# Optimization experiments

Measured on AMD Instinct MI355X. Metric: run time of the kernel, lower is better.

Reference implementation:

```python
import jax, jax.numpy as jnp
import numpy as np


def setup_inputs() -> dict:
    key = jax.random.key(0)
    k1, k2, k3, k4, k5 = jax.random.split(key, 5)
    B, NODES, HID, C, H, W = 16, 64, 128, 256, 128, 128
    inp = {
        "input": jax.random.normal(k1, (1, B, NODES, HID), dtype=jnp.float32),
        "res_feature": jax.random.normal(k2, (B, C, H, W), dtype=jnp.float32),
        "node_fea_for_res": jax.random.normal(k3, (C, 1), dtype=jnp.float32) * 0.05,
        "node_fea_for_hidden": jax.random.normal(k4, (HID, 1), dtype=jnp.float32) * 0.05,
        "weight": jax.random.normal(k5, (HID, C), dtype=jnp.float32) * 0.05,
    }
    return inp


def reference(input, res_feature, node_fea_for_res, node_fea_for_hidden, weight):
    # input: (1, B, nodes, hidden); res_feature: (B, C, H, W)
    b, c, h, w = res_feature.shape
    x = input[0]  # (B, nodes, hidden)

    # res_feature -> (B, HW, C)
    res = res_feature.reshape(b, c, h * w).transpose(0, 2, 1)

    # The torch code expands to (B, HW, nodes, C/hidden) before the matmuls,
    # but the results are constant along the broadcast axis, so compute the
    # reduced projections once and broadcast-add.
    s_res = (res @ node_fea_for_res)[:, :, 0]        # (B, HW)
    s_hid = (x @ node_fea_for_hidden)[:, :, 0]       # (B, nodes)
    scores = s_res[:, :, None] + s_hid[:, None, :]   # (B, HW, nodes)

    attn = jax.nn.softmax(scores, axis=-1)           # softmax over nodes
    new_weight = x @ weight                          # (B, nodes, C)
    feature_out = jnp.einsum('bpn,bnc->bpc', attn, new_weight)  # (B, HW, C)

    feature_out = feature_out.transpose(0, 2, 1).reshape(b, c, h, w)
    return jax.nn.relu(feature_out)
```

## Files before the change

### kernel.cpp

```cpp
#include <hip/hip_runtime.h>

#define BB    16
#define NODES 64
#define HID   128
#define CC    256
#define HWP   16384

__global__ __launch_bounds__(256) void attn_vec_kernel(
    const float* __restrict__ x,
    const float* __restrict__ nfh,
    const float* __restrict__ w,
    float*       __restrict__ vals)
{
    __shared__ float s_part[NODES][4];
    __shared__ float attn[NODES];
    __shared__ float y[HID];

    const int b   = blockIdx.x;
    const int tid = threadIdx.x;

    {
        const int n = tid >> 2;
        const int q = tid & 3;
        const float* xp = x + ((size_t)b * NODES + n) * HID + q * 32;
        const float* fp = nfh + q * 32;
        float acc = 0.f;
        #pragma unroll
        for (int k = 0; k < 32; ++k) acc = fmaf(xp[k], fp[k], acc);
        s_part[n][q] = acc;
    }
    __syncthreads();

    if (tid < NODES) {
        float v = s_part[tid][0] + s_part[tid][1] + s_part[tid][2] + s_part[tid][3];
        float m = v;
        #pragma unroll
        for (int off = 32; off >= 1; off >>= 1)
            m = fmaxf(m, __shfl_xor(m, off, 64));
        float e = __expf(v - m);
        float ssum = e;
        #pragma unroll
        for (int off = 32; off >= 1; off >>= 1)
            ssum += __shfl_xor(ssum, off, 64);
        attn[tid] = e / ssum;
    }
    __syncthreads();

    if (tid < HID) {
        const float* xb = x + (size_t)b * NODES * HID + tid;
        float acc = 0.f;
        #pragma unroll 8
        for (int n = 0; n < NODES; ++n)
            acc = fmaf(attn[n], xb[(size_t)n * HID], acc);
        y[tid] = acc;
    }
    __syncthreads();

    {
        float acc = 0.f;
        #pragma unroll 8
        for (int k = 0; k < HID; ++k)
            acc = fmaf(y[k], w[(size_t)k * CC + tid], acc);
        vals[b * CC + tid] = fmaxf(acc, 0.f);
    }
}

__global__ __launch_bounds__(256) void broadcast_kernel(
    const float* __restrict__ vals,
    float*       __restrict__ out)
{
    const int bc = blockIdx.x;
    const float v = vals[bc];
    const float4 v4 = make_float4(v, v, v, v);
    float4* base = (float4*)(out + (size_t)bc * HWP) + threadIdx.x;
    #pragma unroll
    for (int i = 0; i < HWP / (256 * 4); ++i)
        base[i * 256] = v4;
}

extern "C" void kernel_launch(void* const* d_in, const int* in_sizes, int n_in,
                              void* d_out, int out_size, void* d_ws, size_t ws_size,
                              hipStream_t stream) {
    const float* x   = (const float*)d_in[0];
    const float* nfh = (const float*)d_in[3];
    const float* w   = (const float*)d_in[4];
    float* vals = (float*)d_ws;
    float* out  = (float*)d_out;

    attn_vec_kernel<<<BB, 256, 0, stream>>>(x, nfh, w, vals);
    broadcast_kernel<<<BB * CC, 256, 0, stream>>>(vals, out);
}
```

Measured before the change: 398.1 us.

## Fuse attention vector computation into broadcast kernel, recomputing per output block

Merges the per-batch attention/projection kernel and the broadcast-fill kernel into a single launch. Each (batch, channel) block recomputes the node softmax and the attention-weighted hidden vector, then dot-products it with its own column of the weight matrix before filling its output slice. This removes a kernel launch and the workspace round-trip. In exchange, the softmax and weighted-sum work, plus the reads of x, are repeated in every one of the 4096 blocks instead of once per batch, and that work must finish before each block starts its stores.

```diff
diff --git a/kernel.cpp b/kernel.cpp
--- a/kernel.cpp
+++ b/kernel.cpp
@@ -6,18 +6,21 @@
 #define CC    256
 #define HWP   16384
 
-__global__ __launch_bounds__(256) void attn_vec_kernel(
+__global__ __launch_bounds__(256) void fused_kernel(
     const float* __restrict__ x,
     const float* __restrict__ nfh,
     const float* __restrict__ w,
-    float*       __restrict__ vals)
+    float*       __restrict__ out)
 {
+    const int bc  = blockIdx.x;
+    const int b   = bc >> 8;
+    const int c   = bc & (CC - 1);
+    const int tid = threadIdx.x;
+
     __shared__ float s_part[NODES][4];
     __shared__ float attn[NODES];
-    __shared__ float y[HID];
-
-    const int b   = blockIdx.x;
-    const int tid = threadIdx.x;
+    __shared__ float prod[HID];
+    __shared__ float s_val;
 
     {
         const int n = tid >> 2;
@@ -52,27 +55,22 @@
         #pragma unroll 8
         for (int n = 0; n < NODES; ++n)
             acc = fmaf(attn[n], xb[(size_t)n * HID], acc);
-        y[tid] = acc;
+        prod[tid] = acc * w[(size_t)tid * CC + c];
     }
     __syncthreads();
 
-    {
-        float acc = 0.f;
-        #pragma unroll 8
-        for (int k = 0; k < HID; ++k)
-            acc = fmaf(y[k], w[(size_t)k * CC + tid], acc);
-        vals[b * CC + tid] = fmaxf(acc, 0.f);
+    if (tid < 64) {
+        float v = prod[tid] + prod[tid + 64];
+        #pragma unroll
+        for (int off = 32; off >= 1; off >>= 1)
+            v += __shfl_xor(v, off, 64);
+        if (tid == 0) s_val = fmaxf(v, 0.f);
     }
-}
+    __syncthreads();
 
-__global__ __launch_bounds__(256) void broadcast_kernel(
-    const float* __restrict__ vals,
-    float*       __restrict__ out)
-{
-    const int bc = blockIdx.x;
-    const float v = vals[bc];
-    const float4 v4 = make_float4(v, v, v, v);
-    float4* base = (float4*)(out + (size_t)bc * HWP) + threadIdx.x;
+    const float vv = s_val;
+    const float4 v4 = make_float4(vv, vv, vv, vv);
+    float4* base = (float4*)(out + (size_t)bc * HWP) + tid;
     #pragma unroll
     for (int i = 0; i < HWP / (256 * 4); ++i)
         base[i * 256] = v4;
@@ -84,9 +82,7 @@
     const float* x   = (const float*)d_in[0];
     const float* nfh = (const float*)d_in[3];
     const float* w   = (const float*)d_in[4];
-    float* vals = (float*)d_ws;
-    float* out  = (float*)d_out;
+    float* out = (float*)d_out;
 
-    attn_vec_kernel<<<BB, 256, 0, stream>>>(x, nfh, w, vals);
-    broadcast_kernel<<<BB * CC, 256, 0, stream>>>(vals, out);
+    fused_kernel<<<BB * CC, 256, 0, stream>>>(x, nfh, w, out);
 }
```

New measurement: 395.1 us. About the same (-0.8%).
